# Kernel optimization log

Measured on AMD Instinct MI355X. Metric: run time of the kernel, lower is better.

Reference implementation:

```python
import jax, jax.numpy as jnp
import numpy as np

HIDDEN = 2048
NUM_HEADS = 32
NUM_KV_HEADS = 8
HEAD_DIM = HIDDEN // NUM_HEADS  # 64
GROUP = NUM_HEADS // NUM_KV_HEADS  # 4
B, S = 2, 2048


def setup_inputs() -> dict:
    key = jax.random.key(0)
    ks = jax.random.split(key, 9)
    sc = 0.02
    kv_dim = NUM_KV_HEADS * HEAD_DIM
    return {
        "x": jax.random.normal(ks[0], (B, S, HIDDEN), jnp.float32),
        # weights stored as [in, out] (transpose of torch Linear.weight)
        "Wq": jax.random.normal(ks[1], (HIDDEN, HIDDEN), jnp.float32) * sc,
        "bq": jnp.zeros((HIDDEN,), jnp.float32),
        "Wk": jax.random.normal(ks[2], (HIDDEN, kv_dim), jnp.float32) * sc,
        "bk": jnp.zeros((kv_dim,), jnp.float32),
        "Wv": jax.random.normal(ks[3], (HIDDEN, kv_dim), jnp.float32) * sc,
        "bv": jnp.zeros((kv_dim,), jnp.float32),
        "Wo": jax.random.normal(ks[4], (HIDDEN, HIDDEN), jnp.float32) * sc,
        "bo": jnp.zeros((HIDDEN,), jnp.float32),
    }


def reference(x, Wq, bq, Wk, bk, Wv, bv, Wo, bo):
    b, s, _ = x.shape
    q = (x @ Wq + bq).reshape(b, s, NUM_KV_HEADS, GROUP, HEAD_DIM)
    k = (x @ Wk + bk).reshape(b, s, NUM_KV_HEADS, HEAD_DIM)
    v = (x @ Wv + bv).reshape(b, s, NUM_KV_HEADS, HEAD_DIM)
    scale = 1.0 / jnp.sqrt(jnp.asarray(HEAD_DIM, x.dtype))
    # scores: [b, g(kv heads), r(q per group), s(query), t(key)]
    scores = jnp.einsum("bsgrd,btgd->bgrst", q, k) * scale
    attn = jax.nn.softmax(scores, axis=-1)  # dropout rate 0 -> identity
    out = jnp.einsum("bgrst,btgd->bsgrd", attn, v).reshape(b, s, HIDDEN)
    return out @ Wo + bo
```

## Files before the change

### kernel.cpp

```cpp
#include <hip/hip_runtime.h>

#define HIDDEN 2048
#define NHEADS 32
#define NKV 8
#define HD 64
#define BATCH 2
#define SEQ 2048
#define KVD 512
#define BSZ 4096
#define QKVD 3072

typedef __bf16 bfx8 __attribute__((ext_vector_type(8)));
typedef __bf16 bfx4 __attribute__((ext_vector_type(4)));
typedef float f32x4 __attribute__((ext_vector_type(4)));

__device__ __forceinline__ int sw64(int row, int k) {
    return row * 64 + (k ^ ((row & 7) << 3));
}

__device__ __forceinline__ void gl_lds16(const __bf16* g, __bf16* l) {
    __builtin_amdgcn_global_load_lds(
        (const __attribute__((address_space(1))) unsigned int*)g,
        (__attribute__((address_space(3))) unsigned int*)l, 16, 0, 0);
}

__global__ __launch_bounds__(256) void cvt_bf16(const float* __restrict__ src,
                                                __bf16* __restrict__ dst, int n4) {
    int i = blockIdx.x * 256 + threadIdx.x;
    if (i >= n4) return;
    float4 f = ((const float4*)src)[i];
    bfx4 o = {(__bf16)f.x, (__bf16)f.y, (__bf16)f.z, (__bf16)f.w};
    *(bfx4*)(dst + (size_t)i * 4) = o;
}

__global__ __launch_bounds__(256) void transpose_cvt(const float* __restrict__ src,
                                                     __bf16* __restrict__ dst,
                                                     int R, int C) {
    __shared__ float tile[64][65];
    int t = threadIdx.x;
    int br = blockIdx.y * 64, bc = blockIdx.x * 64;
    {
        int r = t >> 4, c = (t & 15) * 4;
#pragma unroll
        for (int i = 0; i < 4; ++i) {
            float4 v = *(const float4*)(&src[(long)(br + r + i * 16) * C + bc + c]);
            tile[r + i * 16][c + 0] = v.x;
            tile[r + i * 16][c + 1] = v.y;
            tile[r + i * 16][c + 2] = v.z;
            tile[r + i * 16][c + 3] = v.w;
        }
    }
    __syncthreads();
    {
        int d = t >> 2, tt0 = (t & 3) * 16;
        bfx8 o0, o1;
#pragma unroll
        for (int j = 0; j < 8; ++j) o0[j] = (__bf16)tile[tt0 + j][d];
#pragma unroll
        for (int j = 0; j < 8; ++j) o1[j] = (__bf16)tile[tt0 + 8 + j][d];
        *(bfx8*)(&dst[(long)(bc + d) * R + br + tt0]) = o0;
        *(bfx8*)(&dst[(long)(bc + d) * R + br + tt0 + 8]) = o1;
    }
}

__global__ __launch_bounds__(256) void concat_bias(const float* __restrict__ bq,
                                                   const float* __restrict__ bk,
                                                   const float* __restrict__ bv,
                                                   float* __restrict__ o) {
    int i = blockIdx.x * 256 + threadIdx.x;
    if (i >= QKVD) return;
    float v = (i < HIDDEN) ? bq[i] : (i < HIDDEN + KVD ? bk[i - HIDDEN] : bv[i - HIDDEN - KVD]);
    o[i] = v;
}

__global__ __launch_bounds__(256) void transpose_v(const __bf16* __restrict__ qkv,
                                                   __bf16* __restrict__ vt) {
    __shared__ __bf16 tile[64][65];
    int t = threadIdx.x;
    int nb0 = blockIdx.x * 64;
    int bh = blockIdx.y;
    int b = bh >> 3, kv = bh & 7;
    {
        int tt = t >> 2, c0 = (t & 3) * 16;
        const __bf16* p = &qkv[(long)(b * SEQ + nb0 + tt) * QKVD + HIDDEN + KVD + kv * HD + c0];
        bfx8 a0 = *(const bfx8*)(p);
        bfx8 a1 = *(const bfx8*)(p + 8);
#pragma unroll
        for (int j = 0; j < 8; ++j) tile[tt][c0 + j] = a0[j];
#pragma unroll
        for (int j = 0; j < 8; ++j) tile[tt][c0 + 8 + j] = a1[j];
    }
    __syncthreads();
    {
        int d = t >> 2, tt0 = (t & 3) * 16;
        bfx8 o0, o1;
#pragma unroll
        for (int j = 0; j < 8; ++j) o0[j] = tile[tt0 + j][d];
#pragma unroll
        for (int j = 0; j < 8; ++j) o1[j] = tile[tt0 + 8 + j][d];
        __bf16* q = &vt[((long)bh * HD + d) * SEQ + nb0 + tt0];
        *(bfx8*)(q) = o0;
        *(bfx8*)(q + 8) = o1;
    }
}

template <bool OUT_BF16>
__global__ __launch_bounds__(256) void gemm128(const __bf16* __restrict__ A,
                                               const __bf16* __restrict__ Bt,
                                               const float* __restrict__ bias,
                                               void* __restrict__ C,
                                               int M, int N, int K) {
    __shared__ __align__(16) __bf16 As[128 * 32];
    __shared__ __align__(16) __bf16 Bs[128 * 32];
    int t = threadIdx.x;
    int w = t >> 6, lane = t & 63;
    int lrow = lane & 15, quad = lane >> 4;
    long m0 = (long)blockIdx.y * 128, n0 = (long)blockIdx.x * 128;
    int wr = (w >> 1) * 64, wc = (w & 1) * 64;
    f32x4 acc[4][4] = {};
    int srow = t >> 2, scol = (t & 3) * 8;
    const __bf16* Ag = A + (m0 + srow) * (long)K + scol;
    const __bf16* Bg = Bt + (n0 + srow) * (long)K + scol;
    for (int kb = 0; kb < K; kb += 32) {
#pragma unroll
        for (int c = 0; c < 2; ++c) {
            gl_lds16(Ag + (long)c * 64 * K + kb, &As[c * 2048 + w * 512]);
            gl_lds16(Bg + (long)c * 64 * K + kb, &Bs[c * 2048 + w * 512]);
        }
        __syncthreads();
        bfx8 af[4], bfr[4];
#pragma unroll
        for (int i = 0; i < 4; ++i) af[i] = *(const bfx8*)&As[(wr + i * 16 + lrow) * 32 + quad * 8];
#pragma unroll
        for (int j = 0; j < 4; ++j) bfr[j] = *(const bfx8*)&Bs[(wc + j * 16 + lrow) * 32 + quad * 8];
#pragma unroll
        for (int i = 0; i < 4; ++i)
#pragma unroll
            for (int j = 0; j < 4; ++j)
                acc[i][j] = __builtin_amdgcn_mfma_f32_16x16x32_bf16(af[i], bfr[j], acc[i][j], 0, 0, 0);
        __syncthreads();
    }
#pragma unroll
    for (int j = 0; j < 4; ++j) {
        long col = n0 + wc + j * 16 + lrow;
        float bv = bias[col];
#pragma unroll
        for (int i = 0; i < 4; ++i) {
#pragma unroll
            for (int r = 0; r < 4; ++r) {
                long row = m0 + wr + i * 16 + quad * 4 + r;
                float val = acc[i][j][r] + bv;
                if (OUT_BF16)
                    ((__bf16*)C)[row * N + col] = (__bf16)val;
                else
                    ((float*)C)[row * N + col] = val;
            }
        }
    }
}

__global__ __launch_bounds__(256, 2) void attn(const __bf16* __restrict__ QKV,
                                               const __bf16* __restrict__ Vt,
                                               __bf16* __restrict__ O) {
    __shared__ __align__(16) __bf16 Ks[2][64 * 64];
    __shared__ __align__(16) __bf16 Vs[2][64 * 64];
    __shared__ __align__(16) __bf16 Ps[4][64 * 64];
    int t = threadIdx.x;
    int w = t >> 6, lane = t & 63;
    int lrow = lane & 15, quad = lane >> 4;
    int qb = blockIdx.x, bh = blockIdx.y;
    int b = bh >> 5, h = bh & 31, kv = h >> 2;
    int q0 = qb * 256 + w * 64;

    bfx8 qf[4][2];
#pragma unroll
    for (int i = 0; i < 4; ++i)
#pragma unroll
        for (int kk = 0; kk < 2; ++kk)
            qf[i][kk] = *(const bfx8*)(QKV + (long)(b * SEQ + q0 + i * 16 + lrow) * QKVD +
                                       h * HD + kk * 32 + quad * 8);

    int srow = t >> 2, scol = (t & 3) * 8;
    const __bf16* kg = QKV + (long)(b * SEQ + srow) * QKVD + HIDDEN + kv * HD + scol;
    const __bf16* vg = Vt + ((long)(b * NKV + kv) * HD + srow) * SEQ + scol;
#define STAGE_KV(nb, buf)                                                          \
    {                                                                              \
        _Pragma("unroll") for (int c = 0; c < 2; ++c) {                            \
            gl_lds16(kg + (long)(nb)*QKVD + c * 32, &Ks[buf][c * 2048 + w * 512]); \
            gl_lds16(vg + (nb) + c * 32, &Vs[buf][c * 2048 + w * 512]);            \
        }                                                                          \
    }
    STAGE_KV(0, 0);

    f32x4 accO[4][4] = {};
    f32x4 lacc[4] = {};
    bfx8 ones;
#pragma unroll
    for (int j = 0; j < 8; ++j) ones[j] = (__bf16)1.0f;
    const float kScaleLog2e = 0.125f * 1.44269504f;
    __bf16* myPs = &Ps[w][0];

    for (int it = 0; it < SEQ / 64; ++it) {
        __syncthreads();
        if (it + 1 < SEQ / 64) STAGE_KV((it + 1) * 64, (it + 1) & 1);
        const __bf16* Kb = &Ks[it & 1][0];
        const __bf16* Vb = &Vs[it & 1][0];
        bfx8 kb[2][4];
#pragma unroll
        for (int kk = 0; kk < 2; ++kk)
#pragma unroll
            for (int c = 0; c < 4; ++c)
                kb[kk][c] = *(const bfx8*)&Kb[kk * 2048 + c * 512 + lrow * 32 + quad * 8];
#pragma unroll
        for (int i = 0; i < 4; ++i) {
            f32x4 s[4] = {};
#pragma unroll
            for (int kk = 0; kk < 2; ++kk)
#pragma unroll
                for (int c = 0; c < 4; ++c)
                    s[c] = __builtin_amdgcn_mfma_f32_16x16x32_bf16(qf[i][kk], kb[kk][c], s[c], 0, 0, 0);
#pragma unroll
            for (int c = 0; c < 4; ++c)
#pragma unroll
                for (int r = 0; r < 4; ++r) {
                    float p = __builtin_amdgcn_exp2f(s[c][r] * kScaleLog2e);
                    myPs[sw64(i * 16 + quad * 4 + r, c * 16 + lrow)] = (__bf16)p;
                }
        }
#pragma unroll
        for (int kk = 0; kk < 2; ++kk) {
            bfx8 pa[4];
#pragma unroll
            for (int i = 0; i < 4; ++i)
                pa[i] = *(const bfx8*)&myPs[sw64(i * 16 + lrow, kk * 32 + quad * 8)];
#pragma unroll
            for (int c = 0; c < 4; ++c) {
                bfx8 vb = *(const bfx8*)&Vb[kk * 2048 + c * 512 + lrow * 32 + quad * 8];
#pragma unroll
                for (int i = 0; i < 4; ++i)
                    accO[i][c] = __builtin_amdgcn_mfma_f32_16x16x32_bf16(pa[i], vb, accO[i][c], 0, 0, 0);
            }
#pragma unroll
            for (int i = 0; i < 4; ++i)
                lacc[i] = __builtin_amdgcn_mfma_f32_16x16x32_bf16(pa[i], ones, lacc[i], 0, 0, 0);
        }
    }
#pragma unroll
    for (int i = 0; i < 4; ++i) {
        f32x4 inv;
#pragma unroll
        for (int r = 0; r < 4; ++r) inv[r] = 1.0f / lacc[i][r];
#pragma unroll
        for (int c = 0; c < 4; ++c)
#pragma unroll
            for (int r = 0; r < 4; ++r) {
                long row = (long)(b * SEQ + q0 + i * 16 + quad * 4 + r);
                O[row * HIDDEN + h * HD + c * 16 + lrow] = (__bf16)(accO[i][c][r] * inv[r]);
            }
    }
#undef STAGE_KV
}

extern "C" void kernel_launch(void* const* d_in, const int* in_sizes, int n_in,
                              void* d_out, int out_size, void* d_ws, size_t ws_size,
                              hipStream_t stream) {
    const float* x  = (const float*)d_in[0];
    const float* Wq = (const float*)d_in[1];
    const float* bq = (const float*)d_in[2];
    const float* Wk = (const float*)d_in[3];
    const float* bk = (const float*)d_in[4];
    const float* Wv = (const float*)d_in[5];
    const float* bv = (const float*)d_in[6];
    const float* Wo = (const float*)d_in[7];
    const float* bo = (const float*)d_in[8];
    float* out = (float*)d_out;

    __bf16* ws    = (__bf16*)d_ws;
    __bf16* xb    = ws;
    __bf16* wqkvt = xb + (size_t)BSZ * HIDDEN;
    __bf16* wot   = wqkvt + (size_t)QKVD * HIDDEN;
    __bf16* qkv   = wot + (size_t)HIDDEN * HIDDEN;
    __bf16* vt_   = qkv + (size_t)BSZ * QKVD;
    __bf16* ab_   = vt_ + (size_t)BSZ * KVD;
    float*  bqkv  = (float*)(ab_ + (size_t)BSZ * HIDDEN);

    cvt_bf16<<<(BSZ * HIDDEN / 4 + 255) / 256, 256, 0, stream>>>(x, xb, BSZ * HIDDEN / 4);
    transpose_cvt<<<dim3(HIDDEN / 64, HIDDEN / 64), 256, 0, stream>>>(Wq, wqkvt, HIDDEN, HIDDEN);
    transpose_cvt<<<dim3(KVD / 64, HIDDEN / 64), 256, 0, stream>>>(Wk, wqkvt + (size_t)HIDDEN * HIDDEN, HIDDEN, KVD);
    transpose_cvt<<<dim3(KVD / 64, HIDDEN / 64), 256, 0, stream>>>(Wv, wqkvt + (size_t)(HIDDEN + KVD) * HIDDEN, HIDDEN, KVD);
    transpose_cvt<<<dim3(HIDDEN / 64, HIDDEN / 64), 256, 0, stream>>>(Wo, wot, HIDDEN, HIDDEN);
    concat_bias<<<(QKVD + 255) / 256, 256, 0, stream>>>(bq, bk, bv, bqkv);

    gemm128<true><<<dim3(QKVD / 128, BSZ / 128), 256, 0, stream>>>(xb, wqkvt, bqkv, qkv, BSZ, QKVD, HIDDEN);

    transpose_v<<<dim3(SEQ / 64, BATCH * NKV), 256, 0, stream>>>(qkv, vt_);
    attn<<<dim3(SEQ / 256, BATCH * NHEADS), 256, 0, stream>>>(qkv, vt_, ab_);

    gemm128<false><<<dim3(HIDDEN / 128, BSZ / 128), 256, 0, stream>>>(ab_, wot, bo, out, BSZ, HIDDEN, HIDDEN);
}
```

Before: 378.2 us.

## Double-buffer GEMM LDS tiles and fuse weight prep launches into one kernel

The GEMM now keeps two LDS buffers and issues the global-to-LDS loads for the next K step before computing the current one. This drops one barrier per iteration and overlaps load latency with MFMA work, at the cost of doubling shared memory. A launch_bounds occupancy hint is added. The four weight transpose-convert launches and the bias concat are merged into a single prep kernel to cut launch overhead.

New measurement: 332.4 us. 1.14x faster.

```diff
diff --git a/kernel.cpp b/kernel.cpp
--- a/kernel.cpp
+++ b/kernel.cpp
@@ -33,12 +33,11 @@
     *(bfx4*)(dst + (size_t)i * 4) = o;
 }
 
-__global__ __launch_bounds__(256) void transpose_cvt(const float* __restrict__ src,
-                                                     __bf16* __restrict__ dst,
-                                                     int R, int C) {
-    __shared__ float tile[64][65];
-    int t = threadIdx.x;
-    int br = blockIdx.y * 64, bc = blockIdx.x * 64;
+__device__ __forceinline__ void tcvt_tile(const float* __restrict__ src,
+                                          __bf16* __restrict__ dst,
+                                          int R, int C, int tx, int ty,
+                                          float (*tile)[65], int t) {
+    int br = ty * 64, bc = tx * 64;
     {
         int r = t >> 4, c = (t & 15) * 4;
 #pragma unroll
@@ -63,14 +62,37 @@
     }
 }
 
-__global__ __launch_bounds__(256) void concat_bias(const float* __restrict__ bq,
-                                                   const float* __restrict__ bk,
-                                                   const float* __restrict__ bv,
-                                                   float* __restrict__ o) {
-    int i = blockIdx.x * 256 + threadIdx.x;
-    if (i >= QKVD) return;
-    float v = (i < HIDDEN) ? bq[i] : (i < HIDDEN + KVD ? bk[i - HIDDEN] : bv[i - HIDDEN - KVD]);
-    o[i] = v;
+__global__ __launch_bounds__(256) void prep(const float* __restrict__ Wq,
+                                            const float* __restrict__ Wk,
+                                            const float* __restrict__ Wv,
+                                            const float* __restrict__ Wo,
+                                            const float* __restrict__ bq,
+                                            const float* __restrict__ bk,
+                                            const float* __restrict__ bv,
+                                            __bf16* __restrict__ wqkvt,
+                                            __bf16* __restrict__ wot,
+                                            float* __restrict__ bqkv) {
+    __shared__ float tile[64][65];
+    int idx = blockIdx.x, t = threadIdx.x;
+    if (idx < 1024) {
+        tcvt_tile(Wq, wqkvt, HIDDEN, HIDDEN, idx & 31, idx >> 5, tile, t);
+    } else if (idx < 1280) {
+        int l = idx - 1024;
+        tcvt_tile(Wk, wqkvt + (size_t)HIDDEN * HIDDEN, HIDDEN, KVD, l & 7, l >> 3, tile, t);
+    } else if (idx < 1536) {
+        int l = idx - 1280;
+        tcvt_tile(Wv, wqkvt + (size_t)(HIDDEN + KVD) * HIDDEN, HIDDEN, KVD, l & 7, l >> 3, tile, t);
+    } else if (idx < 2560) {
+        int l = idx - 1536;
+        tcvt_tile(Wo, wot, HIDDEN, HIDDEN, l & 31, l >> 5, tile, t);
+    } else {
+        int i = (idx - 2560) * 256 + t;
+        if (i < QKVD) {
+            float v = (i < HIDDEN) ? bq[i]
+                                   : (i < HIDDEN + KVD ? bk[i - HIDDEN] : bv[i - HIDDEN - KVD]);
+            bqkv[i] = v;
+        }
+    }
 }
 
 __global__ __launch_bounds__(256) void transpose_v(const __bf16* __restrict__ qkv,
@@ -105,13 +127,13 @@
 }
 
 template <bool OUT_BF16>
-__global__ __launch_bounds__(256) void gemm128(const __bf16* __restrict__ A,
-                                               const __bf16* __restrict__ Bt,
-                                               const float* __restrict__ bias,
-                                               void* __restrict__ C,
-                                               int M, int N, int K) {
-    __shared__ __align__(16) __bf16 As[128 * 32];
-    __shared__ __align__(16) __bf16 Bs[128 * 32];
+__global__ __launch_bounds__(256, 2) void gemm128(const __bf16* __restrict__ A,
+                                                  const __bf16* __restrict__ Bt,
+                                                  const float* __restrict__ bias,
+                                                  void* __restrict__ C,
+                                                  int M, int N, int K) {
+    __shared__ __align__(16) __bf16 As[2][128 * 32];
+    __shared__ __align__(16) __bf16 Bs[2][128 * 32];
     int t = threadIdx.x;
     int w = t >> 6, lane = t & 63;
     int lrow = lane & 15, quad = lane >> 4;
@@ -121,25 +143,32 @@
     int srow = t >> 2, scol = (t & 3) * 8;
     const __bf16* Ag = A + (m0 + srow) * (long)K + scol;
     const __bf16* Bg = Bt + (n0 + srow) * (long)K + scol;
-    for (int kb = 0; kb < K; kb += 32) {
-#pragma unroll
-        for (int c = 0; c < 2; ++c) {
-            gl_lds16(Ag + (long)c * 64 * K + kb, &As[c * 2048 + w * 512]);
-            gl_lds16(Bg + (long)c * 64 * K + kb, &Bs[c * 2048 + w * 512]);
-        }
+#define STAGE_G(kb, buf)                                                      \
+    {                                                                         \
+        _Pragma("unroll") for (int c = 0; c < 2; ++c) {                       \
+            gl_lds16(Ag + (long)c * 64 * K + (kb), &As[buf][c * 2048 + w * 512]); \
+            gl_lds16(Bg + (long)c * 64 * K + (kb), &Bs[buf][c * 2048 + w * 512]); \
+        }                                                                     \
+    }
+    STAGE_G(0, 0);
+    int nk = K >> 5;
+    for (int it = 0; it < nk; ++it) {
         __syncthreads();
+        if (it + 1 < nk) STAGE_G((it + 1) * 32, (it + 1) & 1);
+        const __bf16* Ab = &As[it & 1][0];
+        const __bf16* Bb = &Bs[it & 1][0];
         bfx8 af[4], bfr[4];
 #pragma unroll
-        for (int i = 0; i < 4; ++i) af[i] = *(const bfx8*)&As[(wr + i * 16 + lrow) * 32 + quad * 8];
-#pragma unroll
-        for (int j = 0; j < 4; ++j) bfr[j] = *(const bfx8*)&Bs[(wc + j * 16 + lrow) * 32 + quad * 8];
+        for (int i = 0; i < 4; ++i) af[i] = *(const bfx8*)&Ab[(wr + i * 16 + lrow) * 32 + quad * 8];
+#pragma unroll
+        for (int j = 0; j < 4; ++j) bfr[j] = *(const bfx8*)&Bb[(wc + j * 16 + lrow) * 32 + quad * 8];
 #pragma unroll
         for (int i = 0; i < 4; ++i)
 #pragma unroll
             for (int j = 0; j < 4; ++j)
                 acc[i][j] = __builtin_amdgcn_mfma_f32_16x16x32_bf16(af[i], bfr[j], acc[i][j], 0, 0, 0);
-        __syncthreads();
-    }
+    }
+#undef STAGE_G
 #pragma unroll
     for (int j = 0; j < 4; ++j) {
         long col = n0 + wc + j * 16 + lrow;
@@ -285,11 +314,8 @@
     float*  bqkv  = (float*)(ab_ + (size_t)BSZ * HIDDEN);
 
     cvt_bf16<<<(BSZ * HIDDEN / 4 + 255) / 256, 256, 0, stream>>>(x, xb, BSZ * HIDDEN / 4);
-    transpose_cvt<<<dim3(HIDDEN / 64, HIDDEN / 64), 256, 0, stream>>>(Wq, wqkvt, HIDDEN, HIDDEN);
-    transpose_cvt<<<dim3(KVD / 64, HIDDEN / 64), 256, 0, stream>>>(Wk, wqkvt + (size_t)HIDDEN * HIDDEN, HIDDEN, KVD);
-    transpose_cvt<<<dim3(KVD / 64, HIDDEN / 64), 256, 0, stream>>>(Wv, wqkvt + (size_t)(HIDDEN + KVD) * HIDDEN, HIDDEN, KVD);
-    transpose_cvt<<<dim3(HIDDEN / 64, HIDDEN / 64), 256, 0, stream>>>(Wo, wot, HIDDEN, HIDDEN);
-    concat_bias<<<(QKVD + 255) / 256, 256, 0, stream>>>(bq, bk, bv, bqkv);
+    prep<<<2560 + (QKVD + 255) / 256, 256, 0, stream>>>(Wq, Wk, Wv, Wo, bq, bk, bv,
+                                                        wqkvt, wot, bqkv);
 
     gemm128<true><<<dim3(QKVD / 128, BSZ / 128), 256, 0, stream>>>(xb, wqkvt, bqkv, qkv, BSZ, QKVD, HIDDEN);
 
```
